# Kernel optimization log

Hardware: AMD Instinct MI355X
Metric: run time of the kernel (lower is better)

## Reference

```python
import jax, jax.numpy as jnp
import numpy as np

B, S, T, E, H, VIN, VOUT = 64, 64, 32, 512, 1024, 32000, 32000


def setup_inputs() -> dict:
    key = jax.random.key(0)
    ks = jax.random.split(key, 12)
    rn = lambda k, shape, s=0.02: jax.random.normal(k, shape, jnp.float32) * s
    return {
        "src": jax.random.randint(ks[0], (B, S), 0, VIN),
        "tgt": jax.random.randint(ks[1], (B, T), 0, VOUT),
        "enc_emb": rn(ks[2], (VIN, E)),
        "dec_emb": rn(ks[3], (VOUT, E)),
        "enc_Wih": rn(ks[4], (4 * H, E)),
        "enc_Whh": rn(ks[5], (4 * H, H)),
        "enc_bih": jnp.zeros((4 * H,), jnp.float32),
        "enc_bhh": jnp.zeros((4 * H,), jnp.float32),
        "dec_Wih": rn(ks[6], (4 * H, E + H)),
        "dec_Whh": rn(ks[7], (4 * H, H)),
        "dec_bih": jnp.zeros((4 * H,), jnp.float32),
        "dec_bhh": jnp.zeros((4 * H,), jnp.float32),
        "attn_W": rn(ks[8], (H, 2 * H)),
        "attn_b": jnp.zeros((H,), jnp.float32),
        "v": jax.random.uniform(ks[9], (H,), jnp.float32),
        "fc_W": rn(ks[10], (VOUT, 2 * H)),
        "fc_b": jnp.zeros((VOUT,), jnp.float32),
    }


def _lstm_cell(x, h, c, Wih, Whh, bih, bhh):
    # torch gate order: i, f, g, o
    gates = x @ Wih.T + bih + h @ Whh.T + bhh
    i, f, g, o = jnp.split(gates, 4, axis=-1)
    c_new = jax.nn.sigmoid(f) * c + jax.nn.sigmoid(i) * jnp.tanh(g)
    h_new = jax.nn.sigmoid(o) * jnp.tanh(c_new)
    return h_new, c_new


def _forward(src, tgt, enc_emb, dec_emb, enc_Wih, enc_Whh, enc_bih, enc_bhh,
             dec_Wih, dec_Whh, dec_bih, dec_bhh, attn_W, attn_b, v, fc_W, fc_b):
    b, s = src.shape
    t_len = tgt.shape[1]
    hdim = enc_Whh.shape[1]

    # ---- encoder (single-layer LSTM, batch_first) ----
    x = enc_emb[src]  # [B,S,E] (dropout=0 in eval)

    def enc_step(carry, x_t):
        h, c = carry
        h, c = _lstm_cell(x_t, h, c, enc_Wih, enc_Whh, enc_bih, enc_bhh)
        return (h, c), h

    h0 = jnp.zeros((b, hdim), x.dtype)
    (h_f, c_f), enc_out_tm = jax.lax.scan(enc_step, (h0, h0), jnp.swapaxes(x, 0, 1))
    enc_out = jnp.swapaxes(enc_out_tm, 0, 1)  # [B,S,H]

    # hidden.detach() in torch
    h_f = jax.lax.stop_gradient(h_f)
    c_f = jax.lax.stop_gradient(c_f)

    # split attn_W for the concat(hidden, enc_out) linear
    Wh, We = attn_W[:, :hdim], attn_W[:, hdim:]
    enc_proj = jnp.einsum('bsh,kh->bsk', enc_out, We)  # hoisted, [B,S,H]

    def dec_step(carry, tok):
        h, c = carry
        emb = dec_emb[tok]  # [B,E]
        # Bahdanau attention: tanh(Linear(cat(h, enc_out))) . v
        energy = jnp.tanh(h @ Wh.T[None] if False else jnp.tanh((h @ Wh.T)[:, None, :] + enc_proj + attn_b))
        energy = jnp.tanh((h @ Wh.T)[:, None, :] + enc_proj + attn_b)  # [B,S,H]
        scores = jnp.einsum('bsh,h->bs', energy, v)
        a = jax.nn.softmax(scores, axis=1)
        context = jnp.einsum('bs,bsh->bh', a, enc_out)  # [B,H]
        rnn_in = jnp.concatenate([emb, context], axis=-1)
        h_new, c_new = _lstm_cell(rnn_in, h, c, dec_Wih, dec_Whh, dec_bih, dec_bhh)
        logits = jnp.concatenate([h_new, context], axis=-1) @ fc_W.T + fc_b
        return (h_new, c_new), logits

    # teacher_forcing_ratio = 1.0 -> input at step t is tgt[:, t-1]
    toks_tm = jnp.swapaxes(tgt[:, : t_len - 1], 0, 1)  # [T-1, B]
    _, logits_tm = jax.lax.scan(dec_step, (h_f, c_f), toks_tm)  # [T-1,B,V]
    logits = jnp.swapaxes(logits_tm, 0, 1)  # [B,T-1,V]
    zeros0 = jnp.zeros((b, 1, fc_W.shape[0]), logits.dtype)
    return jnp.concatenate([zeros0, logits], axis=1)  # [B,T,V]


def reference(src, tgt, enc_emb, dec_emb, enc_Wih, enc_Whh, enc_bih, enc_bhh,
              dec_Wih, dec_Whh, dec_bih, dec_bhh, attn_W, attn_b, v, fc_W, fc_b):
    return _forward(src, tgt, enc_emb, dec_emb, enc_Wih, enc_Whh, enc_bih, enc_bhh,
                    dec_Wih, dec_Whh, dec_bih, dec_bhh, attn_W, attn_b, v, fc_W, fc_b)
```

## Files before the change

kernel.cpp:

```cpp
#include <hip/hip_runtime.h>
#include <hip/hip_bf16.h>

typedef __bf16 bf16x8 __attribute__((ext_vector_type(8)));
typedef float  f32x4  __attribute__((ext_vector_type(4)));
typedef _Float16 h16x8 __attribute__((ext_vector_type(8)));

__device__ __forceinline__ unsigned short f2b(float f) {
    union { float f; unsigned u; } w; w.f = f;
    unsigned u = w.u + 0x7FFF + ((w.u >> 16) & 1);
    return (unsigned short)(u >> 16);
}
__device__ __forceinline__ float tanhfast(float x) {
    float e = __expf(2.0f * x);
    return 1.0f - 2.0f / (e + 1.0f);
}

__device__ __forceinline__ void stU(unsigned* p, unsigned v) {
    __hip_atomic_store(p, v, __ATOMIC_RELAXED, __HIP_MEMORY_SCOPE_AGENT);
}
__device__ __forceinline__ void stF(float* p, float v) {
    __hip_atomic_store(p, v, __ATOMIC_RELAXED, __HIP_MEMORY_SCOPE_AGENT);
}
__device__ __forceinline__ int ldI(const int* p) {
    return __hip_atomic_load((int*)p, __ATOMIC_RELAXED, __HIP_MEMORY_SCOPE_AGENT);
}
__device__ __forceinline__ void stI(int* p, int v) {
    __hip_atomic_store(p, v, __ATOMIC_RELAXED, __HIP_MEMORY_SCOPE_AGENT);
}

#define GLD16(g, l) __builtin_amdgcn_global_load_lds( \
    (const __attribute__((address_space(1))) void*)(g), \
    (__attribute__((address_space(3))) void*)(l), 16, 0, 0)

#define SLOT_STRIDE 16
#define NPOLL 256

__device__ __forceinline__ void gbar(int* slots, int* gen, int target) {
    asm volatile("s_waitcnt vmcnt(0)" ::: "memory");
    __syncthreads();
    if (blockIdx.x == 0) {
        if (threadIdx.x == 0) stI(slots, target);
        if (threadIdx.x < NPOLL) {
            while (ldI(slots + threadIdx.x * SLOT_STRIDE) < target)
                __builtin_amdgcn_s_sleep(1);
        }
        __syncthreads();
        if (threadIdx.x == 0) stI(gen, target);
    } else {
        if (threadIdx.x == 0) {
            stI(slots + blockIdx.x * SLOT_STRIDE, target);
            while (ldI(gen) < target)
                __builtin_amdgcn_s_sleep(1);
        }
        __syncthreads();
    }
}

__device__ __forceinline__ void mac16L(const unsigned short* A, const bf16x8* BL,
                                       f32x4& acc) {
    bf16x8 a[16];
#pragma unroll
    for (int kk = 0; kk < 16; ++kk) a[kk] = *(const bf16x8*)(A + kk * 32);
#pragma unroll
    for (int kk = 0; kk < 16; ++kk)
        acc = __builtin_amdgcn_mfma_f32_16x16x32_bf16(a[kk], BL[kk * 64], acc, 0, 0, 0);
}
__device__ __forceinline__ void mac4L(const unsigned short* A, const bf16x8* BL,
                                      f32x4& acc) {
    bf16x8 a[4];
#pragma unroll
    for (int kk = 0; kk < 4; ++kk) a[kk] = *(const bf16x8*)(A + kk * 32);
#pragma unroll
    for (int kk = 0; kk < 4; ++kk)
        acc = __builtin_amdgcn_mfma_f32_16x16x32_bf16(a[kk], BL[kk * 64], acc, 0, 0, 0);
}


__global__ void k_gather(const float* __restrict__ emb, const int* __restrict__ tok,
                         unsigned short* __restrict__ out, int L, int ldtok) {
    long total = (long)L * 64 * 128;
    for (long i = (long)blockIdx.x * blockDim.x + threadIdx.x; i < total;
         i += (long)gridDim.x * blockDim.x) {
        int  e4 = (int)(i & 127);
        long r  = i >> 7;
        int  t  = (int)(r >> 6), b = (int)(r & 63);
        int  tk = tok[b * ldtok + t];
        float4 v = *(const float4*)(emb + (long)tk * 512 + e4 * 4);
        ushort4 o; o.x = f2b(v.x); o.y = f2b(v.y); o.z = f2b(v.z); o.w = f2b(v.w);
        *(ushort4*)(out + r * 512 + e4 * 4) = o;
    }
}

__global__ void k_conv(const float* __restrict__ in, unsigned short* __restrict__ out,
                       long N_, int K_, int ldin, int col0, int ldout, int outcol0, int reorder) {
    long total = N_ * (K_ >> 2);
    int kq = K_ >> 2;
    for (long i = (long)blockIdx.x * blockDim.x + threadIdx.x; i < total;
         i += (long)gridDim.x * blockDim.x) {
        long n = i / kq;
        int  k4 = (int)(i - n * kq) * 4;
        long row = reorder ? (long)((n & 3) * 1024 + (n >> 2)) : n;
        float4 v = *(const float4*)(in + row * ldin + col0 + k4);
        ushort4 o; o.x = f2b(v.x); o.y = f2b(v.y); o.z = f2b(v.z); o.w = f2b(v.w);
        *(ushort4*)(out + n * ldout + outcol0 + k4) = o;
    }
}

__global__ void k_bias(const float* __restrict__ b1, const float* __restrict__ b2,
                       float* __restrict__ out) {
    int n = blockIdx.x * blockDim.x + threadIdx.x;
    if (n < 4096) {
        int row = (n & 3) * 1024 + (n >> 2);
        out[n] = b1[row] + b2[row];
    }
}

__global__ void k_zero0(float* __restrict__ out) {
    long total = 64L * 8000;
    for (long i = (long)blockIdx.x * blockDim.x + threadIdx.x; i < total;
         i += (long)gridDim.x * blockDim.x) {
        int b = (int)(i / 8000), q = (int)(i % 8000);
        float4 z = {0.f, 0.f, 0.f, 0.f};
        *(float4*)(out + (long)b * 1024000 + q * 4) = z;
    }
}

template<int BM, int BN, int WGM, int WGN, int FM, int FN>
__device__ __forceinline__ void gemm_core(
    const unsigned short* __restrict__ A, int lda,
    const unsigned short* __restrict__ B, int ldb,
    long m0, long n0, int K,
    unsigned short* As, unsigned short* Bs,
    f32x4 (&acc)[FM][FN])
{
    const int tid  = threadIdx.x;
    const int lane = tid & 63;
    const int wave = tid >> 6;
    const int wm = wave / WGN;
    const int wn = wave % WGN;
    const int srow = lane >> 2;
    const int scol = (lane & 3) * 8;
    const int frow = lane & 15;
    const int fcol = (lane >> 4) * 8;

    for (int k0 = 0; k0 < K; k0 += 32) {
        __syncthreads();
        for (int c = wave; c < BM / 16; c += 4) {
            const unsigned short* g = A + (m0 + c * 16 + srow) * (long)lda + k0 + scol;
            GLD16(g, As + c * 512);
        }
        for (int c = wave; c < BN / 16; c += 4) {
            const unsigned short* g = B + (n0 + c * 16 + srow) * (long)ldb + k0 + scol;
            GLD16(g, Bs + c * 512);
        }
        __syncthreads();
        bf16x8 af[FM], bfr[FN];
#pragma unroll
        for (int m = 0; m < FM; ++m)
            af[m] = *(const bf16x8*)(As + ((wm * FM + m) * 16 + frow) * 32 + fcol);
#pragma unroll
        for (int n = 0; n < FN; ++n)
            bfr[n] = *(const bf16x8*)(Bs + ((wn * FN + n) * 16 + frow) * 32 + fcol);
#pragma unroll
        for (int m = 0; m < FM; ++m)
#pragma unroll
            for (int n = 0; n < FN; ++n)
                acc[m][n] = __builtin_amdgcn_mfma_f32_16x16x32_bf16(af[m], bfr[n], acc[m][n], 0, 0, 0);
    }
}

template<int BM, int BN, int WGM, int WGN, int FM, int FN, int MODE>
__global__ __launch_bounds__(256) void k_gemm(
    const unsigned short* __restrict__ A, int lda,
    const unsigned short* __restrict__ B, int ldb,
    float* __restrict__ C, long ldc, const float* __restrict__ bias,
    int M, int N, int K, int Mreal)
{
    __shared__ __align__(16) unsigned short As[BM * 32];
    __shared__ __align__(16) unsigned short Bs[BN * 32];
    long m0 = (long)blockIdx.y * BM;
    long n0 = (long)blockIdx.x * BN;
    f32x4 acc[FM][FN] = {};
    gemm_core<BM, BN, WGM, WGN, FM, FN>(A, lda, B, ldb, m0, n0, K, As, Bs, acc);

    const int lane = threadIdx.x & 63;
    const int wave = threadIdx.x >> 6;
    const int wm = wave / WGN, wn = wave % WGN;
#pragma unroll
    for (int n = 0; n < FN; ++n) {
        long col = n0 + wn * FN * 16 + n * 16 + (lane & 15);
        float bv = bias ? bias[col] : 0.0f;
#pragma unroll
        for (int m = 0; m < FM; ++m) {
            int rl = wm * FM * 16 + m * 16 + (lane >> 4) * 4;
#pragma unroll
            for (int q = 0; q < 4; ++q) {
                long r = m0 + rl + q;
                float val = acc[m][n][q] + bv;
                if (MODE == 0) {
                    C[r * ldc + col] = val;
                } else {
                    ((_Float16*)C)[r * ldc + col] = (_Float16)val;
                }
            }
        }
    }
}

template<int BM, int BN, int WGN, int FM, int FN>
__global__ __launch_bounds__(256) void k_fc(
    const unsigned short* __restrict__ A, int lda,
    const unsigned short* __restrict__ B, int ldb,
    float* __restrict__ C, long ldc, const float* __restrict__ bias,
    int K, int Mreal)
{
    __shared__ __align__(16) unsigned short As[2][BM * 32];
    __shared__ __align__(16) unsigned short Bs[2][BN * 32];
    int bid = blockIdx.x;
    int n = (bid & 7) * 32 + (bid >> 7);
    int m = (bid >> 3) & 15;
    if (n >= 250) return;
    long m0 = (long)m * BM, n0 = (long)n * BN;
    const int tid = threadIdx.x, lane = tid & 63, wave = tid >> 6;
    const int wm = wave / WGN, wn = wave % WGN;
    const int srow = lane >> 2, scol = (lane & 3) * 8;
    const int frow = lane & 15, fcol = (lane >> 4) * 8;
    f32x4 acc[FM][FN] = {};

#define FC_STAGE(buf, k0) \
    { for (int c = wave; c < BM / 16; c += 4) \
          GLD16(A + (m0 + c * 16 + srow) * (long)lda + (k0) + scol, As[buf] + c * 512); \
      for (int c = wave; c < BN / 16; c += 4) \
          GLD16(B + (n0 + c * 16 + srow) * (long)ldb + (k0) + scol, Bs[buf] + c * 512); }

    FC_STAGE(0, 0);
    asm volatile("s_waitcnt vmcnt(0)" ::: "memory");
    __syncthreads();
    const int NT = K / 32;
    for (int t = 0; t < NT; ++t) {
        int cur = t & 1;
        if (t + 1 < NT) FC_STAGE(cur ^ 1, (t + 1) * 32);
        bf16x8 af[FM], bfr[FN];
#pragma unroll
        for (int mm = 0; mm < FM; ++mm)
            af[mm] = *(const bf16x8*)(As[cur] + ((wm * FM + mm) * 16 + frow) * 32 + fcol);
#pragma unroll
        for (int nn = 0; nn < FN; ++nn)
            bfr[nn] = *(const bf16x8*)(Bs[cur] + ((wn * FN + nn) * 16 + frow) * 32 + fcol);
#pragma unroll
        for (int mm = 0; mm < FM; ++mm)
#pragma unroll
            for (int nn = 0; nn < FN; ++nn)
                acc[mm][nn] = __builtin_amdgcn_mfma_f32_16x16x32_bf16(af[mm], bfr[nn], acc[mm][nn], 0, 0, 0);
        asm volatile("s_waitcnt vmcnt(0)" ::: "memory");
        __syncthreads();
    }
#undef FC_STAGE
#pragma unroll
    for (int nn = 0; nn < FN; ++nn) {
        long col = n0 + wn * FN * 16 + nn * 16 + (lane & 15);
        float bv = bias[col];
#pragma unroll
        for (int mm = 0; mm < FM; ++mm) {
            int rl = wm * FM * 16 + mm * 16 + (lane >> 4) * 4;
#pragma unroll
            for (int q = 0; q < 4; ++q) {
                long r = m0 + rl + q;
                if (r < Mreal) {
                    long orow = (r & 63) * 32 + (r >> 6) + 1;
                    C[orow * ldc + col] = acc[mm][nn][q] + bv;
                }
            }
        }
    }
}

__global__ __launch_bounds__(512, 2) void k_enc(
    const unsigned short* __restrict__ W,
    const float* __restrict__ pre,
    unsigned short* __restrict__ hsl,
    unsigned short* __restrict__ enc_out,
    unsigned short* __restrict__ eoT,
    unsigned short* __restrict__ hS0,
    float* __restrict__ cspill,
    int* slots, int* gen)
{
    __shared__ __align__(16) unsigned short WL[16 * 1024];
    __shared__ float gs[64 * 16];
    const int blk = blockIdx.x, tid = threadIdx.x;
    const int lane = tid & 63, wave = tid >> 6;
    const int rt = wave >> 1, kh = wave & 1;
    const int n0 = blk * 16;
    const int grow = (rt * 16 + (lane >> 4) * 4) * 16 + (lane & 15);
    const int pb = tid >> 1, pjl = (tid & 1) * 2;
    const int jg = blk * 4 + pjl;
    for (int i = tid; i < 2048; i += 512) {
        int r = i & 15, k8 = i >> 4;
        ((bf16x8*)WL)[k8 * 16 + r] = *(const bf16x8*)(W + (long)(n0 + r) * 1024 + k8 * 8);
    }
    const bf16x8* BL = (const bf16x8*)WL + ((long)kh * 64 + (lane >> 4)) * 16 + (lane & 15);
    float c0 = 0.f, c1 = 0.f;
    float4 pr0 = {}, pr1 = {};
    if (tid < 128) {
        pr0 = *(const float4*)(pre + (long)pb * 4096 + n0 + pjl * 4);
        pr1 = *(const float4*)(pre + (long)pb * 4096 + n0 + pjl * 4 + 4);
    }
    __syncthreads();
    int bt = 0;
    for (int t = 0; t < 64; ++t) {
        const unsigned short* Ar = hsl + (long)t * 65536
            + (long)(rt * 16 + (lane & 15)) * 1024 + kh * 512 + (lane >> 4) * 8;
        f32x4 acc = {};
        mac16L(Ar, BL, acc);
        if (kh == 0) {
#pragma unroll
            for (int q = 0; q < 4; ++q) gs[grow + q * 16] = acc[q];
        }
        __syncthreads();
        if (kh == 1) {
#pragma unroll
            for (int q = 0; q < 4; ++q) atomicAdd(&gs[grow + q * 16], acc[q]);
        }
        __syncthreads();
        if (tid < 128) {
            float4 gA = *(const float4*)(gs + pb * 16 + pjl * 4);
            float4 gB = *(const float4*)(gs + pb * 16 + pjl * 4 + 4);
            float h0v, h1v;
            {
                float gi = gA.x + pr0.x, gf = gA.y + pr0.y, gg = gA.z + pr0.z, go = gA.w + pr0.w;
                float i_ = 1.f / (1.f + __expf(-gi)), f_ = 1.f / (1.f + __expf(-gf));
                float g_ = tanhfast(gg), o_ = 1.f / (1.f + __expf(-go));
                c0 = f_ * c0 + i_ * g_; h0v = o_ * tanhfast(c0);
            }
            {
                float gi = gB.x + pr1.x, gf = gB.y + pr1.y, gg = gB.z + pr1.z, go = gB.w + pr1.w;
                float i_ = 1.f / (1.f + __expf(-gi)), f_ = 1.f / (1.f + __expf(-gf));
                float g_ = tanhfast(gg), o_ = 1.f / (1.f + __expf(-go));
                c1 = f_ * c1 + i_ * g_; h1v = o_ * tanhfast(c1);
            }
            unsigned short hb0 = f2b(h0v), hb1 = f2b(h1v);
            unsigned pk = (unsigned)hb0 | ((unsigned)hb1 << 16);
            stU((unsigned*)(hsl + (long)(t + 1) * 65536 + (long)pb * 1024 + jg), pk);
            *(unsigned*)(enc_out + ((long)pb * 64 + t) * 1024 + jg) = pk;
            eoT[((long)pb * 1024 + jg) * 64 + t]     = hb0;
            eoT[((long)pb * 1024 + jg + 1) * 64 + t] = hb1;
            if (t < 63) {
                pr0 = *(const float4*)(pre + (long)(t + 1) * 262144 + (long)pb * 4096 + n0 + pjl * 4);
                pr1 = *(const float4*)(pre + (long)(t + 1) * 262144 + (long)pb * 4096 + n0 + pjl * 4 + 4);
            } else {
                *(unsigned*)(hS0 + (long)pb * 1024 + jg) = pk;
                cspill[(long)pb * 1024 + jg]     = c0;
                cspill[(long)pb * 1024 + jg + 1] = c1;
            }
        }
        gbar(slots, gen, ++bt);
    }
}

__global__ __launch_bounds__(512, 2) void k_dec(
    const unsigned short* __restrict__ Wh,
    const unsigned short* __restrict__ Wc,
    const float* __restrict__ pre,
    const _Float16* __restrict__ proj16,
    const unsigned short* __restrict__ eoT,
    const float* __restrict__ v,
    const float* __restrict__ cspill,
    unsigned short* __restrict__ hS,
    unsigned short* __restrict__ ctxS,
    float* __restrict__ qS,
    unsigned short* __restrict__ fcin,
    int* slots, int* gen)
{
    __shared__ __align__(16) unsigned short WcL[16 * 2048];
    __shared__ __align__(16) unsigned short WhL[16 * 1024];
    __shared__ float gs[64 * 16];
    __shared__ float qv[1024], vv[1024];
    __shared__ float sc[64], al[64];
    const int blk = blockIdx.x, tid = threadIdx.x;
    const int lane = tid & 63, wave = tid >> 6;
    const int rt = wave >> 1, kh = wave & 1;
    const int n0 = blk * 16;
    const int nq = blk >> 2, mt = blk & 3;
    const int grow = (rt * 16 + (lane >> 4) * 4) * 16 + (lane & 15);
    const int pb = tid >> 1, pjl = (tid & 1) * 2;
    const int jg = blk * 4 + pjl;
    for (int i = tid; i < 4096; i += 512) {
        int r = i & 15, k8 = i >> 4;
        ((bf16x8*)WcL)[k8 * 16 + r] = *(const bf16x8*)(Wc + (long)(n0 + r) * 2048 + k8 * 8);
    }
    for (int i = tid; i < 2048; i += 512) {
        int r = i & 15, k8 = i >> 4;
        ((bf16x8*)WhL)[k8 * 16 + r] = *(const bf16x8*)(Wh + (long)(nq * 16 + r) * 1024 + k8 * 8);
    }
    const bf16x8* BLc = (const bf16x8*)WcL + ((long)kh * 128 + (lane >> 4)) * 16 + (lane & 15);
    const bf16x8* BLq = (const bf16x8*)WhL + ((long)wave * 16 + (lane >> 4)) * 16 + (lane & 15);
    if (tid < 256) {
        float4 v4 = *(const float4*)(v + tid * 4);
        *(float4*)(vv + tid * 4) = v4;
    }
    float c0 = 0.f, c1 = 0.f;
    if (tid < 128) {
        c0 = cspill[(long)pb * 1024 + jg];
        c1 = cspill[(long)pb * 1024 + jg + 1];
    }
    __syncthreads();
    int bt = 0;
    for (int t = 0; t < 31; ++t) {
        const unsigned short* hSt   = hS   + (long)t * 65536;
        const unsigned short* ctxSt = ctxS + (long)t * 65536;
        float4 pr0 = {}, pr1 = {};
        if (tid < 128) {
            pr0 = *(const float4*)(pre + (long)t * 262144 + (long)pb * 4096 + n0 + pjl * 4);
            pr1 = *(const float4*)(pre + (long)t * 262144 + (long)pb * 4096 + n0 + pjl * 4 + 4);
        }
        {
            if (tid < 256) gs[tid] = 0.f;
            __syncthreads();
            const unsigned short* Ar = hSt + (long)(mt * 16 + (lane & 15)) * 1024
                                           + wave * 128 + (lane >> 4) * 8;
            f32x4 qa = {};
            mac4L(Ar, BLq, qa);
#pragma unroll
            for (int q = 0; q < 4; ++q)
                atomicAdd(&gs[((lane >> 4) * 4 + q) * 16 + (lane & 15)], qa[q]);
            __syncthreads();
            if (tid < 256)
                stF(qS + (long)t * 65536 + (long)(mt * 16 + (tid >> 4)) * 1024
                        + nq * 16 + (tid & 15), gs[tid]);
        }
        gbar(slots, gen, ++bt);
        if (blk < 64) {
            const int b = blk;
            if (tid < 256)
                *(float4*)(qv + tid * 4) =
                    *(const float4*)(qS + (long)t * 65536 + (long)b * 1024 + tid * 4);
            __syncthreads();
            int s = tid >> 3, part = tid & 7;
            const h16x8* pp = (const h16x8*)(proj16 + ((long)b * 64 + s) * 1024 + part * 128);
            float a_ = 0.f;
#pragma unroll 4
            for (int d = 0; d < 16; ++d) {
                h16x8 pv = pp[d];
                int h = part * 128 + d * 8;
#pragma unroll
                for (int j = 0; j < 8; ++j)
                    a_ += vv[h + j] * tanhfast(qv[h + j] + (float)pv[j]);
            }
            a_ += __shfl_xor(a_, 1);
            a_ += __shfl_xor(a_, 2);
            a_ += __shfl_xor(a_, 4);
            if (part == 0) sc[s] = a_;
            __syncthreads();
            if (tid < 64) {
                float x = sc[tid], mx = x;
                for (int o = 32; o; o >>= 1) mx = fmaxf(mx, __shfl_xor(mx, o));
                float e = __expf(x - mx), su = e;
                for (int o = 32; o; o >>= 1) su += __shfl_xor(su, o);
                al[tid] = e / su;
            }
            __syncthreads();
            int h0 = tid * 2;
            const bf16x8* ep = (const bf16x8*)(eoT + ((long)b * 1024 + h0) * 64);
            bf16x8 e[16];
#pragma unroll
            for (int c8 = 0; c8 < 16; ++c8) e[c8] = ep[c8];
            float cacc[2];
#pragma unroll
            for (int r = 0; r < 2; ++r) {
                float s_ = 0.f;
#pragma unroll
                for (int c8 = 0; c8 < 8; ++c8) {
                    bf16x8 v8 = e[r * 8 + c8];
#pragma unroll
                    for (int jj = 0; jj < 8; ++jj)
                        s_ += al[c8 * 8 + jj] * (float)v8[jj];
                }
                cacc[r] = s_;
            }
            unsigned pk0 = (unsigned)f2b(cacc[0]) | ((unsigned)f2b(cacc[1]) << 16);
            stU((unsigned*)(ctxS + (long)t * 65536 + (long)b * 1024 + h0), pk0);
            *(unsigned*)(fcin + ((long)t * 64 + b) * 2048 + 1024 + h0) = pk0;
        }
        gbar(slots, gen, ++bt);
        {
            const unsigned short* Asrc = (kh ? ctxSt : hSt)
                + (long)(rt * 16 + (lane & 15)) * 1024 + (lane >> 4) * 8;
            f32x4 acc = {};
            mac16L(Asrc,       BLc,        acc);
            mac16L(Asrc + 512, BLc + 1024, acc);
            if (kh == 0) {
#pragma unroll
                for (int q = 0; q < 4; ++q) gs[grow + q * 16] = acc[q];
            }
            __syncthreads();
            if (kh == 1) {
#pragma unroll
                for (int q = 0; q < 4; ++q) atomicAdd(&gs[grow + q * 16], acc[q]);
            }
            __syncthreads();
            if (tid < 128) {
                float4 gA = *(const float4*)(gs + pb * 16 + pjl * 4);
                float4 gB = *(const float4*)(gs + pb * 16 + pjl * 4 + 4);
                float h0v, h1v;
                {
                    float gi = gA.x + pr0.x, gf = gA.y + pr0.y, gg = gA.z + pr0.z, go = gA.w + pr0.w;
                    float i_ = 1.f / (1.f + __expf(-gi)), f_ = 1.f / (1.f + __expf(-gf));
                    float g_ = tanhfast(gg), o_ = 1.f / (1.f + __expf(-go));
                    c0 = f_ * c0 + i_ * g_; h0v = o_ * tanhfast(c0);
                }
                {
                    float gi = gB.x + pr1.x, gf = gB.y + pr1.y, gg = gB.z + pr1.z, go = gB.w + pr1.w;
                    float i_ = 1.f / (1.f + __expf(-gi)), f_ = 1.f / (1.f + __expf(-gf));
                    float g_ = tanhfast(gg), o_ = 1.f / (1.f + __expf(-go));
                    c1 = f_ * c1 + i_ * g_; h1v = o_ * tanhfast(c1);
                }
                unsigned pk = (unsigned)f2b(h0v) | ((unsigned)f2b(h1v) << 16);
                stU((unsigned*)(hS + (long)(t + 1) * 65536 + (long)pb * 1024 + jg), pk);
                *(unsigned*)(fcin + ((long)t * 64 + pb) * 2048 + jg) = pk;
            }
        }
        gbar(slots, gen, ++bt);
    }
}

extern "C" void kernel_launch(void* const* d_in, const int* in_sizes, int n_in,
                              void* d_out, int out_size, void* d_ws, size_t ws_size,
                              hipStream_t stream) {
    const int*   src     = (const int*)d_in[0];
    const int*   tgt     = (const int*)d_in[1];
    const float* enc_emb = (const float*)d_in[2];
    const float* dec_emb = (const float*)d_in[3];
    const float* enc_Wih = (const float*)d_in[4];
    const float* enc_Whh = (const float*)d_in[5];
    const float* enc_bih = (const float*)d_in[6];
    const float* enc_bhh = (const float*)d_in[7];
    const float* dec_Wih = (const float*)d_in[8];
    const float* dec_Whh = (const float*)d_in[9];
    const float* dec_bih = (const float*)d_in[10];
    const float* dec_bhh = (const float*)d_in[11];
    const float* attn_W  = (const float*)d_in[12];
    const float* attn_b  = (const float*)d_in[13];
    const float* vvec    = (const float*)d_in[14];
    const float* fc_W    = (const float*)d_in[15];
    const float* fc_b    = (const float*)d_in[16];
    float* out = (float*)d_out;

    char* ws = (char*)d_ws;
    size_t off = 0;
    auto alloc = [&](size_t bytes) -> char* {
        off = (off + 255) & ~(size_t)255;
        char* p = ws + off; off += bytes; return p;
    };
    unsigned short* wX      = (unsigned short*)alloc(4096UL * 512 * 2);
    unsigned short* weWih   = (unsigned short*)alloc(4096UL * 512 * 2);
    unsigned short* weWhh   = (unsigned short*)alloc(4096UL * 1024 * 2);
    float*          ebias   = (float*)alloc(4096UL * 4);
    float*          pre_enc = (float*)alloc(4096UL * 4096 * 4);
    unsigned short* enc_out = (unsigned short*)alloc(4096UL * 1024 * 2);
    unsigned short* eoT     = (unsigned short*)alloc(64UL * 1024 * 64 * 2);
    unsigned short* wWe     = (unsigned short*)alloc(1024UL * 1024 * 2);
    unsigned short* wWh     = (unsigned short*)alloc(1024UL * 1024 * 2);
    _Float16*       proj16  = (_Float16*)alloc(4096UL * 1024 * 2);
    float*          cbuf    = (float*)alloc(64UL * 1024 * 4);
    unsigned short* demb    = (unsigned short*)alloc(2048UL * 512 * 2);
    unsigned short* wDemb   = (unsigned short*)alloc(4096UL * 512 * 2);
    unsigned short* wCat    = (unsigned short*)alloc(4096UL * 2048 * 2);
    float*          dbias   = (float*)alloc(4096UL * 4);
    float*          pre_dec = (float*)alloc(2048UL * 4096 * 4);
    unsigned short* fcin    = (unsigned short*)alloc(2048UL * 2048 * 2);
    unsigned short* wFc     = (unsigned short*)alloc(32000UL * 2048 * 2);
    unsigned short* hslE    = (unsigned short*)alloc(65UL * 65536 * 2);
    unsigned short* hS      = (unsigned short*)alloc(32UL * 65536 * 2);
    unsigned short* ctxS    = (unsigned short*)alloc(32UL * 65536 * 2);
    float*          qS      = (float*)alloc(32UL * 65536 * 4);
    int*            bar     = (int*)alloc(65536);
    (void)ws_size; (void)in_sizes; (void)n_in; (void)out_size;

    int* slotsE = bar;
    int* genE   = bar + 4096;
    int* slotsD = bar + 8192;
    int* genD   = bar + 12288;

    hipMemsetAsync(bar, 0, 65536, stream);
    hipMemsetAsync(hslE, 0, 65536UL * 2, stream);
    k_zero0<<<512, 256, 0, stream>>>(out);

    k_gather<<<2048, 256, 0, stream>>>(enc_emb, src, wX, 64, 64);
    k_gather<<<1024, 256, 0, stream>>>(dec_emb, tgt, demb, 31, 32);
    k_conv<<<2048, 256, 0, stream>>>(enc_Wih, weWih, 4096, 512, 512, 0, 512, 0, 1);
    k_conv<<<2048, 256, 0, stream>>>(enc_Whh, weWhh, 4096, 1024, 1024, 0, 1024, 0, 1);
    k_conv<<<2048, 256, 0, stream>>>(dec_Wih, wDemb, 4096, 512, 1536, 0, 512, 0, 1);
    k_conv<<<2048, 256, 0, stream>>>(dec_Whh, wCat, 4096, 1024, 1024, 0, 2048, 0, 1);
    k_conv<<<2048, 256, 0, stream>>>(dec_Wih, wCat, 4096, 1024, 1536, 512, 2048, 1024, 1);
    k_conv<<<2048, 256, 0, stream>>>(attn_W, wWh, 1024, 1024, 2048, 0, 1024, 0, 0);
    k_conv<<<2048, 256, 0, stream>>>(attn_W, wWe, 1024, 1024, 2048, 1024, 1024, 0, 0);
    k_conv<<<4096, 256, 0, stream>>>(fc_W, wFc, 32000, 2048, 2048, 0, 2048, 0, 0);
    k_bias<<<16, 256, 0, stream>>>(enc_bih, enc_bhh, ebias);
    k_bias<<<16, 256, 0, stream>>>(dec_bih, dec_bhh, dbias);

    k_gemm<128,128,2,2,4,4,0><<<dim3(32, 32), 256, 0, stream>>>(
        wX, 512, weWih, 512, pre_enc, 4096, ebias, 4096, 4096, 512, 4096);
    k_gemm<128,128,2,2,4,4,0><<<dim3(32, 16), 256, 0, stream>>>(
        demb, 512, wDemb, 512, pre_dec, 4096, dbias, 2048, 4096, 512, 2048);

    k_enc<<<256, 512, 0, stream>>>(weWhh, pre_enc, hslE, enc_out, eoT,
                                   hS, cbuf, slotsE, genE);

    k_gemm<128,128,2,2,4,4,2><<<dim3(8, 32), 256, 0, stream>>>(
        enc_out, 1024, wWe, 1024, (float*)proj16, 1024, attn_b, 4096, 1024, 1024, 4096);

    k_dec<<<256, 512, 0, stream>>>(wWh, wCat, pre_dec, proj16, eoT, vvec, cbuf,
                                   hS, ctxS, qS, fcin, slotsD, genD);

    k_fc<128,128,2,4,4><<<dim3(4096), 256, 0, stream>>>(
        fcin, 2048, wFc, 2048, out, 32000, fc_b, 2048, 1984);
}
```

Before: 2.327 ms.

## Compute attention query per batch block locally, removing a grid barrier per decoder step

```diff
diff --git a/kernel.cpp b/kernel.cpp
--- a/kernel.cpp
+++ b/kernel.cpp
@@ -10,15 +10,15 @@
     unsigned u = w.u + 0x7FFF + ((w.u >> 16) & 1);
     return (unsigned short)(u >> 16);
 }
+__device__ __forceinline__ float b2f(unsigned short s) {
+    union { unsigned u; float f; } w; w.u = ((unsigned)s) << 16; return w.f;
+}
 __device__ __forceinline__ float tanhfast(float x) {
     float e = __expf(2.0f * x);
     return 1.0f - 2.0f / (e + 1.0f);
 }
 
 __device__ __forceinline__ void stU(unsigned* p, unsigned v) {
-    __hip_atomic_store(p, v, __ATOMIC_RELAXED, __HIP_MEMORY_SCOPE_AGENT);
-}
-__device__ __forceinline__ void stF(float* p, float v) {
     __hip_atomic_store(p, v, __ATOMIC_RELAXED, __HIP_MEMORY_SCOPE_AGENT);
 }
 __device__ __forceinline__ int ldI(const int* p) {
@@ -63,15 +63,6 @@
     for (int kk = 0; kk < 16; ++kk) a[kk] = *(const bf16x8*)(A + kk * 32);
 #pragma unroll
     for (int kk = 0; kk < 16; ++kk)
-        acc = __builtin_amdgcn_mfma_f32_16x16x32_bf16(a[kk], BL[kk * 64], acc, 0, 0, 0);
-}
-__device__ __forceinline__ void mac4L(const unsigned short* A, const bf16x8* BL,
-                                      f32x4& acc) {
-    bf16x8 a[4];
-#pragma unroll
-    for (int kk = 0; kk < 4; ++kk) a[kk] = *(const bf16x8*)(A + kk * 32);
-#pragma unroll
-    for (int kk = 0; kk < 4; ++kk)
         acc = __builtin_amdgcn_mfma_f32_16x16x32_bf16(a[kk], BL[kk * 64], acc, 0, 0, 0);
 }
 
@@ -103,6 +94,21 @@
         float4 v = *(const float4*)(in + row * ldin + col0 + k4);
         ushort4 o; o.x = f2b(v.x); o.y = f2b(v.y); o.z = f2b(v.z); o.w = f2b(v.w);
         *(ushort4*)(out + n * ldout + outcol0 + k4) = o;
+    }
+}
+
+__global__ void k_conv16(const float* __restrict__ in, _Float16* __restrict__ out,
+                         long N_, int K_, int ldin, int col0) {
+    long total = N_ * (K_ >> 2);
+    int kq = K_ >> 2;
+    for (long i = (long)blockIdx.x * blockDim.x + threadIdx.x; i < total;
+         i += (long)gridDim.x * blockDim.x) {
+        long n = i / kq;
+        int  k4 = (int)(i - n * kq) * 4;
+        float4 v = *(const float4*)(in + n * ldin + col0 + k4);
+        _Float16* o = out + n * K_ + k4;
+        o[0] = (_Float16)v.x; o[1] = (_Float16)v.y;
+        o[2] = (_Float16)v.z; o[3] = (_Float16)v.w;
     }
 }
 
@@ -358,7 +364,7 @@
 }
 
 __global__ __launch_bounds__(512, 2) void k_dec(
-    const unsigned short* __restrict__ Wh,
+    const _Float16* __restrict__ Wh16,
     const unsigned short* __restrict__ Wc,
     const float* __restrict__ pre,
     const _Float16* __restrict__ proj16,
@@ -367,20 +373,17 @@
     const float* __restrict__ cspill,
     unsigned short* __restrict__ hS,
     unsigned short* __restrict__ ctxS,
-    float* __restrict__ qS,
     unsigned short* __restrict__ fcin,
     int* slots, int* gen)
 {
     __shared__ __align__(16) unsigned short WcL[16 * 2048];
-    __shared__ __align__(16) unsigned short WhL[16 * 1024];
     __shared__ float gs[64 * 16];
-    __shared__ float qv[1024], vv[1024];
+    __shared__ float hv[1024], qv[1024], vv[1024];
     __shared__ float sc[64], al[64];
     const int blk = blockIdx.x, tid = threadIdx.x;
     const int lane = tid & 63, wave = tid >> 6;
     const int rt = wave >> 1, kh = wave & 1;
     const int n0 = blk * 16;
-    const int nq = blk >> 2, mt = blk & 3;
     const int grow = (rt * 16 + (lane >> 4) * 4) * 16 + (lane & 15);
     const int pb = tid >> 1, pjl = (tid & 1) * 2;
     const int jg = blk * 4 + pjl;
@@ -388,12 +391,7 @@
         int r = i & 15, k8 = i >> 4;
         ((bf16x8*)WcL)[k8 * 16 + r] = *(const bf16x8*)(Wc + (long)(n0 + r) * 2048 + k8 * 8);
     }
-    for (int i = tid; i < 2048; i += 512) {
-        int r = i & 15, k8 = i >> 4;
-        ((bf16x8*)WhL)[k8 * 16 + r] = *(const bf16x8*)(Wh + (long)(nq * 16 + r) * 1024 + k8 * 8);
-    }
     const bf16x8* BLc = (const bf16x8*)WcL + ((long)kh * 128 + (lane >> 4)) * 16 + (lane & 15);
-    const bf16x8* BLq = (const bf16x8*)WhL + ((long)wave * 16 + (lane >> 4)) * 16 + (lane & 15);
     if (tid < 256) {
         float4 v4 = *(const float4*)(v + tid * 4);
         *(float4*)(vv + tid * 4) = v4;
@@ -413,27 +411,30 @@
             pr0 = *(const float4*)(pre + (long)t * 262144 + (long)pb * 4096 + n0 + pjl * 4);
             pr1 = *(const float4*)(pre + (long)t * 262144 + (long)pb * 4096 + n0 + pjl * 4 + 4);
         }
-        {
-            if (tid < 256) gs[tid] = 0.f;
-            __syncthreads();
-            const unsigned short* Ar = hSt + (long)(mt * 16 + (lane & 15)) * 1024
-                                           + wave * 128 + (lane >> 4) * 8;
-            f32x4 qa = {};
-            mac4L(Ar, BLq, qa);
-#pragma unroll
-            for (int q = 0; q < 4; ++q)
-                atomicAdd(&gs[((lane >> 4) * 4 + q) * 16 + (lane & 15)], qa[q]);
-            __syncthreads();
-            if (tid < 256)
-                stF(qS + (long)t * 65536 + (long)(mt * 16 + (tid >> 4)) * 1024
-                        + nq * 16 + (tid & 15), gs[tid]);
-        }
-        gbar(slots, gen, ++bt);
         if (blk < 64) {
             const int b = blk;
-            if (tid < 256)
-                *(float4*)(qv + tid * 4) =
-                    *(const float4*)(qS + (long)t * 65536 + (long)b * 1024 + tid * 4);
+            {
+                unsigned pk = *(const unsigned*)(hSt + (long)b * 1024 + tid * 2);
+                hv[tid * 2]     = b2f((unsigned short)(pk & 0xFFFF));
+                hv[tid * 2 + 1] = b2f((unsigned short)(pk >> 16));
+            }
+            __syncthreads();
+            {
+                float a0 = 0.f, a1 = 0.f;
+                const h16x8* w0 = (const h16x8*)(Wh16 + (long)(tid * 2) * 1024);
+                const h16x8* w1 = (const h16x8*)(Wh16 + (long)(tid * 2 + 1) * 1024);
+#pragma unroll 4
+                for (int k8 = 0; k8 < 128; ++k8) {
+                    h16x8 x0 = w0[k8], x1 = w1[k8];
+                    const float* hp = hv + k8 * 8;
+#pragma unroll
+                    for (int j = 0; j < 8; ++j) {
+                        a0 += hp[j] * (float)x0[j];
+                        a1 += hp[j] * (float)x1[j];
+                    }
+                }
+                qv[tid * 2] = a0; qv[tid * 2 + 1] = a1;
+            }
             __syncthreads();
             int s = tid >> 3, part = tid & 7;
             const h16x8* pp = (const h16x8*)(proj16 + ((long)b * 64 + s) * 1024 + part * 128);
@@ -559,7 +560,7 @@
     unsigned short* enc_out = (unsigned short*)alloc(4096UL * 1024 * 2);
     unsigned short* eoT     = (unsigned short*)alloc(64UL * 1024 * 64 * 2);
     unsigned short* wWe     = (unsigned short*)alloc(1024UL * 1024 * 2);
-    unsigned short* wWh     = (unsigned short*)alloc(1024UL * 1024 * 2);
+    _Float16*       wWh16   = (_Float16*)alloc(1024UL * 1024 * 2);
     _Float16*       proj16  = (_Float16*)alloc(4096UL * 1024 * 2);
     float*          cbuf    = (float*)alloc(64UL * 1024 * 4);
     unsigned short* demb    = (unsigned short*)alloc(2048UL * 512 * 2);
@@ -572,7 +573,6 @@
     unsigned short* hslE    = (unsigned short*)alloc(65UL * 65536 * 2);
     unsigned short* hS      = (unsigned short*)alloc(32UL * 65536 * 2);
     unsigned short* ctxS    = (unsigned short*)alloc(32UL * 65536 * 2);
-    float*          qS      = (float*)alloc(32UL * 65536 * 4);
     int*            bar     = (int*)alloc(65536);
     (void)ws_size; (void)in_sizes; (void)n_in; (void)out_size;
 
@@ -592,7 +592,7 @@
     k_conv<<<2048, 256, 0, stream>>>(dec_Wih, wDemb, 4096, 512, 1536, 0, 512, 0, 1);
     k_conv<<<2048, 256, 0, stream>>>(dec_Whh, wCat, 4096, 1024, 1024, 0, 2048, 0, 1);
     k_conv<<<2048, 256, 0, stream>>>(dec_Wih, wCat, 4096, 1024, 1536, 512, 2048, 1024, 1);
-    k_conv<<<2048, 256, 0, stream>>>(attn_W, wWh, 1024, 1024, 2048, 0, 1024, 0, 0);
+    k_conv16<<<2048, 256, 0, stream>>>(attn_W, wWh16, 1024, 1024, 2048, 0);
     k_conv<<<2048, 256, 0, stream>>>(attn_W, wWe, 1024, 1024, 2048, 1024, 1024, 0, 0);
     k_conv<<<4096, 256, 0, stream>>>(fc_W, wFc, 32000, 2048, 2048, 0, 2048, 0, 0);
     k_bias<<<16, 256, 0, stream>>>(enc_bih, enc_bhh, ebias);
@@ -609,8 +609,8 @@
     k_gemm<128,128,2,2,4,4,2><<<dim3(8, 32), 256, 0, stream>>>(
         enc_out, 1024, wWe, 1024, (float*)proj16, 1024, attn_b, 4096, 1024, 1024, 4096);
 
-    k_dec<<<256, 512, 0, stream>>>(wWh, wCat, pre_dec, proj16, eoT, vvec, cbuf,
-                                   hS, ctxS, qS, fcin, slotsD, genD);
+    k_dec<<<256, 512, 0, stream>>>(wWh16, wCat, pre_dec, proj16, eoT, vvec, cbuf,
+                                   hS, ctxS, fcin, slotsD, genD);
 
     k_fc<128,128,2,4,4><<<dim3(4096), 256, 0, stream>>>(
         fcin, 2048, wFc, 2048, out, 32000, fc_b, 2048, 1984);
```

Result: slower. 4.047 ms (+73.9%).

## Merge small prep kernels and split decoder attention across all blocks

Applied to the files above, without the earlier changes.

```diff
diff --git a/kernel.cpp b/kernel.cpp
--- a/kernel.cpp
+++ b/kernel.cpp
@@ -76,13 +76,17 @@
 }
 
 
-__global__ void k_gather(const float* __restrict__ emb, const int* __restrict__ tok,
-                         unsigned short* __restrict__ out, int L, int ldtok) {
-    long total = (long)L * 64 * 128;
-    for (long i = (long)blockIdx.x * blockDim.x + threadIdx.x; i < total;
+__global__ void k_gather2(const float* __restrict__ enc_emb, const int* __restrict__ src,
+                          const float* __restrict__ dec_emb, const int* __restrict__ tgt,
+                          unsigned short* __restrict__ wX, unsigned short* __restrict__ demb) {
+    const long T1 = 64L * 64 * 128, T2 = 31L * 64 * 128;
+    for (long i = (long)blockIdx.x * blockDim.x + threadIdx.x; i < T1 + T2;
          i += (long)gridDim.x * blockDim.x) {
-        int  e4 = (int)(i & 127);
-        long r  = i >> 7;
+        const float* emb; const int* tok; unsigned short* out; int ldtok; long j;
+        if (i < T1) { emb = enc_emb; tok = src; out = wX; ldtok = 64; j = i; }
+        else        { emb = dec_emb; tok = tgt; out = demb; ldtok = 32; j = i - T1; }
+        int  e4 = (int)(j & 127);
+        long r  = j >> 7;
         int  t  = (int)(r >> 6), b = (int)(r & 63);
         int  tk = tok[b * ldtok + t];
         float4 v = *(const float4*)(emb + (long)tk * 512 + e4 * 4);
@@ -106,12 +110,34 @@
     }
 }
 
-__global__ void k_bias(const float* __restrict__ b1, const float* __restrict__ b2,
-                       float* __restrict__ out) {
+__global__ void k_attnw(const float* __restrict__ attn_W,
+                        unsigned short* __restrict__ wWh,
+                        unsigned short* __restrict__ wWe) {
+    long total = 1024L * 256;
+    for (long i = (long)blockIdx.x * blockDim.x + threadIdx.x; i < total;
+         i += (long)gridDim.x * blockDim.x) {
+        long n = i >> 8;
+        int  k4 = (int)(i & 255) * 4;
+        float4 a = *(const float4*)(attn_W + n * 2048 + k4);
+        float4 b = *(const float4*)(attn_W + n * 2048 + 1024 + k4);
+        ushort4 oa; oa.x = f2b(a.x); oa.y = f2b(a.y); oa.z = f2b(a.z); oa.w = f2b(a.w);
+        ushort4 ob; ob.x = f2b(b.x); ob.y = f2b(b.y); ob.z = f2b(b.z); ob.w = f2b(b.w);
+        *(ushort4*)(wWh + n * 1024 + k4) = oa;
+        *(ushort4*)(wWe + n * 1024 + k4) = ob;
+    }
+}
+
+__global__ void k_bias2(const float* __restrict__ e1, const float* __restrict__ e2,
+                        const float* __restrict__ d1, const float* __restrict__ d2,
+                        float* __restrict__ eb, float* __restrict__ db) {
     int n = blockIdx.x * blockDim.x + threadIdx.x;
     if (n < 4096) {
         int row = (n & 3) * 1024 + (n >> 2);
-        out[n] = b1[row] + b2[row];
+        eb[n] = e1[row] + e2[row];
+    } else if (n < 8192) {
+        int m = n - 4096;
+        int row = (m & 3) * 1024 + (m >> 2);
+        db[m] = d1[row] + d2[row];
     }
 }
 
@@ -381,6 +407,7 @@
     const int rt = wave >> 1, kh = wave & 1;
     const int n0 = blk * 16;
     const int nq = blk >> 2, mt = blk & 3;
+    const int ab = blk >> 2, qt = blk & 3;
     const int grow = (rt * 16 + (lane >> 4) * 4) * 16 + (lane & 15);
     const int pb = tid >> 1, pjl = (tid & 1) * 2;
     const int jg = blk * 4 + pjl;
@@ -429,8 +456,8 @@
                         + nq * 16 + (tid & 15), gs[tid]);
         }
         gbar(slots, gen, ++bt);
-        if (blk < 64) {
-            const int b = blk;
+        {
+            const int b = ab;
             if (tid < 256)
                 *(float4*)(qv + tid * 4) =
                     *(const float4*)(qS + (long)t * 65536 + (long)b * 1024 + tid * 4);
@@ -459,27 +486,29 @@
                 al[tid] = e / su;
             }
             __syncthreads();
-            int h0 = tid * 2;
-            const bf16x8* ep = (const bf16x8*)(eoT + ((long)b * 1024 + h0) * 64);
-            bf16x8 e[16];
-#pragma unroll
-            for (int c8 = 0; c8 < 16; ++c8) e[c8] = ep[c8];
-            float cacc[2];
-#pragma unroll
-            for (int r = 0; r < 2; ++r) {
-                float s_ = 0.f;
-#pragma unroll
-                for (int c8 = 0; c8 < 8; ++c8) {
-                    bf16x8 v8 = e[r * 8 + c8];
-#pragma unroll
-                    for (int jj = 0; jj < 8; ++jj)
-                        s_ += al[c8 * 8 + jj] * (float)v8[jj];
+            if (tid < 128) {
+                int h0 = qt * 256 + tid * 2;
+                const bf16x8* ep = (const bf16x8*)(eoT + ((long)b * 1024 + h0) * 64);
+                bf16x8 e[16];
+#pragma unroll
+                for (int c8 = 0; c8 < 16; ++c8) e[c8] = ep[c8];
+                float cacc[2];
+#pragma unroll
+                for (int r = 0; r < 2; ++r) {
+                    float s_ = 0.f;
+#pragma unroll
+                    for (int c8 = 0; c8 < 8; ++c8) {
+                        bf16x8 v8 = e[r * 8 + c8];
+#pragma unroll
+                        for (int jj = 0; jj < 8; ++jj)
+                            s_ += al[c8 * 8 + jj] * (float)v8[jj];
+                    }
+                    cacc[r] = s_;
                 }
-                cacc[r] = s_;
-            }
-            unsigned pk0 = (unsigned)f2b(cacc[0]) | ((unsigned)f2b(cacc[1]) << 16);
-            stU((unsigned*)(ctxS + (long)t * 65536 + (long)b * 1024 + h0), pk0);
-            *(unsigned*)(fcin + ((long)t * 64 + b) * 2048 + 1024 + h0) = pk0;
+                unsigned pk0 = (unsigned)f2b(cacc[0]) | ((unsigned)f2b(cacc[1]) << 16);
+                stU((unsigned*)(ctxS + (long)t * 65536 + (long)b * 1024 + h0), pk0);
+                *(unsigned*)(fcin + ((long)t * 64 + b) * 2048 + 1024 + h0) = pk0;
+            }
         }
         gbar(slots, gen, ++bt);
         {
@@ -585,18 +614,15 @@
     hipMemsetAsync(hslE, 0, 65536UL * 2, stream);
     k_zero0<<<512, 256, 0, stream>>>(out);
 
-    k_gather<<<2048, 256, 0, stream>>>(enc_emb, src, wX, 64, 64);
-    k_gather<<<1024, 256, 0, stream>>>(dec_emb, tgt, demb, 31, 32);
+    k_gather2<<<2048, 256, 0, stream>>>(enc_emb, src, dec_emb, tgt, wX, demb);
     k_conv<<<2048, 256, 0, stream>>>(enc_Wih, weWih, 4096, 512, 512, 0, 512, 0, 1);
     k_conv<<<2048, 256, 0, stream>>>(enc_Whh, weWhh, 4096, 1024, 1024, 0, 1024, 0, 1);
     k_conv<<<2048, 256, 0, stream>>>(dec_Wih, wDemb, 4096, 512, 1536, 0, 512, 0, 1);
     k_conv<<<2048, 256, 0, stream>>>(dec_Whh, wCat, 4096, 1024, 1024, 0, 2048, 0, 1);
     k_conv<<<2048, 256, 0, stream>>>(dec_Wih, wCat, 4096, 1024, 1536, 512, 2048, 1024, 1);
-    k_conv<<<2048, 256, 0, stream>>>(attn_W, wWh, 1024, 1024, 2048, 0, 1024, 0, 0);
-    k_conv<<<2048, 256, 0, stream>>>(attn_W, wWe, 1024, 1024, 2048, 1024, 1024, 0, 0);
+    k_attnw<<<2048, 256, 0, stream>>>(attn_W, wWh, wWe);
     k_conv<<<4096, 256, 0, stream>>>(fc_W, wFc, 32000, 2048, 2048, 0, 2048, 0, 0);
-    k_bias<<<16, 256, 0, stream>>>(enc_bih, enc_bhh, ebias);
-    k_bias<<<16, 256, 0, stream>>>(dec_bih, dec_bhh, dbias);
+    k_bias2<<<32, 256, 0, stream>>>(enc_bih, enc_bhh, dec_bih, dec_bhh, ebias, dbias);
 
     k_gemm<128,128,2,2,4,4,0><<<dim3(32, 32), 256, 0, stream>>>(
         wX, 512, weWih, 512, pre_enc, 4096, ebias, 4096, 4096, 512, 4096);
```

Result: no change. 2.291 ms (-1.6%).
